# Kernel optimization log

Hardware: AMD Instinct MI355X
Metric: run time of the kernel (lower is better)

Reference implementation:

```python
import jax, jax.numpy as jnp
import numpy as np

N_NODES, N_EDGES, IN_F = 20000, 320000, 64
H1, H2 = 2, 2          # attn heads per GATv2 layer
D1, D2 = 128, 128      # gnn_size per layer
NM = [128, 128]        # nodemlp hidden sizes
EM = [512, 256]        # edgemlp hidden sizes
OUT_F = 1
NEG_SLOPE = 0.2


def _lin_init(key, fan_in, fan_out):
    kw, kb = jax.random.split(key)
    s = 1.0 / np.sqrt(fan_in)
    return (jax.random.uniform(kw, (fan_in, fan_out), jnp.float32, -s, s),
            jax.random.uniform(kb, (fan_out,), jnp.float32, -s, s))


def setup_inputs() -> dict:
    key = jax.random.key(0)
    ks = jax.random.split(key, 16)
    x = jax.random.normal(ks[0], (N_NODES, IN_F), jnp.float32)
    src = jax.random.randint(ks[1], (N_EDGES,), 0, N_NODES, jnp.int32)
    dst = jax.random.randint(ks[2], (N_EDGES,), 0, N_NODES, jnp.int32)
    # NodeMLP
    nw0, nb0 = _lin_init(ks[3], IN_F, NM[0])
    nw1, nb1 = _lin_init(ks[4], NM[0], NM[1])
    # GATv2 layer 1 (in=IN_F -> H1*D1)
    g1ws, g1bs = _lin_init(ks[5], IN_F, H1 * D1)
    g1wd, g1bd = _lin_init(ks[6], IN_F, H1 * D1)
    g1a = jax.random.normal(ks[7], (H1, D1), jnp.float32) * (1.0 / np.sqrt(D1))
    # GATv2 layer 2 (in=H1*D1 -> H2*D2)
    g2ws, g2bs = _lin_init(ks[8], H1 * D1, H2 * D2)
    g2wd, g2bd = _lin_init(ks[9], H1 * D1, H2 * D2)
    g2a = jax.random.normal(ks[10], (H2, D2), jnp.float32) * (1.0 / np.sqrt(D2))
    # EdgeMLP: in = 2*(NM[-1] + H2*D2) = 768
    e_in = 2 * (NM[-1] + H2 * D2)
    ew0, eb0 = _lin_init(ks[11], e_in, EM[0])
    ew1, eb1 = _lin_init(ks[12], EM[0], EM[1])
    ew2, eb2 = _lin_init(ks[13], EM[1], OUT_F)
    return dict(x=x, src=src, dst=dst,
                nw0=nw0, nb0=nb0, nw1=nw1, nb1=nb1,
                g1ws=g1ws, g1bs=g1bs, g1wd=g1wd, g1bd=g1bd, g1a=g1a,
                g2ws=g2ws, g2bs=g2bs, g2wd=g2wd, g2bd=g2bd, g2a=g2a,
                ew0=ew0, eb0=eb0, ew1=ew1, eb1=eb1, ew2=ew2, eb2=eb2)


def _segment_softmax(logits, dst, n):
    # logits: (E, H); softmax over edges sharing the same dst node
    m = jax.ops.segment_max(logits, dst, num_segments=n)
    e = jnp.exp(logits - m[dst])
    s = jax.ops.segment_sum(e, dst, num_segments=n)
    return e / s[dst]


def _gatv2(h, src, dst, ws, bs, wd, bd, attn, heads, dim, n):
    fs = (h @ ws + bs).reshape(n, heads, dim)   # fc_src
    fd = (h @ wd + bd).reshape(n, heads, dim)   # fc_dst
    e = jax.nn.leaky_relu(fs[src] + fd[dst], NEG_SLOPE)      # (E,H,D)
    logits = jnp.einsum('ehd,hd->eh', e, attn)               # (E,H)
    a = _segment_softmax(logits, dst, n)                      # (E,H)
    out = jax.ops.segment_sum(a[..., None] * fs[src], dst, num_segments=n)
    return jax.nn.relu(out).reshape(n, heads * dim)           # flatten heads


def reference(x, src, dst,
              nw0, nb0, nw1, nb1,
              g1ws, g1bs, g1wd, g1bd, g1a,
              g2ws, g2bs, g2wd, g2bd, g2a,
              ew0, eb0, ew1, eb1, ew2, eb2):
    n = x.shape[0]
    # NodeMLP (dropout=0 -> identity)
    h1 = jax.nn.relu(x @ nw0 + nb0)
    h1 = jax.nn.relu(h1 @ nw1 + nb1)
    # GCN: two GATv2Conv layers with relu activation, heads flattened
    h2 = _gatv2(x, src, dst, g1ws, g1bs, g1wd, g1bd, g1a, H1, D1, n)
    h2 = _gatv2(h2, src, dst, g2ws, g2bs, g2wd, g2bd, g2a, H2, D2, n)
    # EdgeMLP: gather src/dst, concat, MLP (relu before every layer but first)
    h = jnp.concatenate([h1[src], h1[dst], h2[src], h2[dst]], axis=1)  # (E,768)
    h = h @ ew0 + eb0
    h = jax.nn.relu(h) @ ew1 + eb1
    h = jax.nn.relu(h) @ ew2 + eb2
    return h  # (E, 1) edge scores
```

## Files before the change

### kernel.cpp

```cpp
#include <hip/hip_runtime.h>
#include <hip/hip_bf16.h>

constexpr int N_NODES = 20000;
constexpr int N_EDGES = 320000;

typedef _Float16 half8 __attribute__((ext_vector_type(8)));
typedef _Float16 half4 __attribute__((ext_vector_type(4)));
typedef float    f32x16 __attribute__((ext_vector_type(16)));

__device__ __forceinline__ float lrelu(float x) { return x > 0.f ? x : 0.2f * x; }

__global__ void hist_kernel(const int* __restrict__ dst, int* __restrict__ counts) {
    int e = blockIdx.x * 256 + threadIdx.x;
    if (e < N_EDGES) atomicAdd(&counts[dst[e]], 1);
}

__global__ void scan_all_kernel(const int* __restrict__ counts,
                                int* __restrict__ row_off, int* __restrict__ cursor) {
    __shared__ int ps[1024];
    const int t = threadIdx.x;
    const int base = t * 20;
    int loc[20];
    int sum = 0;
#pragma unroll
    for (int i = 0; i < 20; ++i) {
        const int idx = base + i;
        const int v = (idx < N_NODES) ? counts[idx] : 0;
        loc[i] = sum;
        sum += v;
    }
    ps[t] = sum;
    __syncthreads();
    for (int off = 1; off < 1024; off <<= 1) {
        const int v = (t >= off) ? ps[t - off] : 0;
        __syncthreads();
        ps[t] += v;
        __syncthreads();
    }
    const int ex = ps[t] - sum;
#pragma unroll
    for (int i = 0; i < 20; ++i) {
        const int idx = base + i;
        if (idx < N_NODES) {
            row_off[idx] = ex + loc[i];
            cursor[idx]  = ex + loc[i];
        }
    }
    if (t == 0) row_off[N_NODES] = N_EDGES;
}

__global__ void scatter_kernel(const int* __restrict__ src, const int* __restrict__ dst,
                               int* __restrict__ cursor, int* __restrict__ eidx,
                               int* __restrict__ srcs) {
    int e = blockIdx.x * 256 + threadIdx.x;
    if (e < N_EDGES) {
        int p = atomicAdd(&cursor[dst[e]], 1);
        eidx[p] = e;
        srcs[p] = src[e];
    }
}

template <int K, int M>
__device__ __forceinline__ void pack_one(int idx, const float* __restrict__ W,
                                         int r1, int k1, int r2, int joff, int ldw,
                                         _Float16* __restrict__ H,
                                         _Float16* __restrict__ L) {
    const int l  = idx & 63;
    const int t  = (idx >> 6) % (M / 32);
    const int s  = (idx >> 6) / (M / 32);
    const int j  = joff + t * 32 + (l & 31);
    const int kb = s * 16 + (l >> 5) * 8;
    half8 vh, vl;
#pragma unroll
    for (int i = 0; i < 8; ++i) {
        const int k    = kb + i;
        const int rrow = (k < k1) ? (r1 + k) : (r2 + (k - k1));
        const float w  = W[(size_t)rrow * ldw + j];
        const _Float16 h = (_Float16)w;
        vh[i] = h;
        vl[i] = (_Float16)(w - (float)h);
    }
    reinterpret_cast<half8*>(H)[idx] = vh;
    reinterpret_cast<half8*>(L)[idx] = vl;
}

constexpr int OFF_W1  = 0;
constexpr int OFF_G1S = 16384;
constexpr int OFF_G1D = 18432;
constexpr int OFF_G2S = 20480;
constexpr int OFF_G2D = 28672;
constexpr int OFF_SW0 = 36864;
constexpr int OFF_SW1 = 49152;
constexpr int OFF_DW0 = 61440;
constexpr int OFF_DW1 = 73728;
constexpr int OFF_N0  = 86016;
constexpr int OFF_N1  = 87040;
constexpr int PACK_TOT = 89088;

struct PackIn {
    const float *ew1, *g1ws, *g1wd, *g2ws, *g2wd, *ew0, *nw0, *nw1;
    _Float16 *H, *L;
};

__global__ void prepack_all_kernel(PackIn a) {
    const int idx = blockIdx.x * 256 + threadIdx.x;
    if (idx >= PACK_TOT) return;
    _Float16* H = a.H;
    _Float16* L = a.L;
    if (idx < OFF_G1S)
        pack_one<512, 256>(idx - OFF_W1, a.ew1, 0, 512, 0, 0, 256,
                           H + OFF_W1 * 8, L + OFF_W1 * 8);
    else if (idx < OFF_G1D)
        pack_one<64, 256>(idx - OFF_G1S, a.g1ws, 0, 64, 0, 0, 256,
                          H + OFF_G1S * 8, L + OFF_G1S * 8);
    else if (idx < OFF_G2S)
        pack_one<64, 256>(idx - OFF_G1D, a.g1wd, 0, 64, 0, 0, 256,
                          H + OFF_G1D * 8, L + OFF_G1D * 8);
    else if (idx < OFF_G2D)
        pack_one<256, 256>(idx - OFF_G2S, a.g2ws, 0, 256, 0, 0, 256,
                           H + OFF_G2S * 8, L + OFF_G2S * 8);
    else if (idx < OFF_SW0)
        pack_one<256, 256>(idx - OFF_G2D, a.g2wd, 0, 256, 0, 0, 256,
                           H + OFF_G2D * 8, L + OFF_G2D * 8);
    else if (idx < OFF_SW1)
        pack_one<384, 256>(idx - OFF_SW0, a.ew0, 0, 128, 256, 0, 512,
                           H + OFF_SW0 * 8, L + OFF_SW0 * 8);
    else if (idx < OFF_DW0)
        pack_one<384, 256>(idx - OFF_SW1, a.ew0, 0, 128, 256, 256, 512,
                           H + OFF_SW1 * 8, L + OFF_SW1 * 8);
    else if (idx < OFF_DW1)
        pack_one<384, 256>(idx - OFF_DW0, a.ew0, 128, 128, 512, 0, 512,
                           H + OFF_DW0 * 8, L + OFF_DW0 * 8);
    else if (idx < OFF_N0)
        pack_one<384, 256>(idx - OFF_DW1, a.ew0, 128, 128, 512, 256, 512,
                           H + OFF_DW1 * 8, L + OFF_DW1 * 8);
    else if (idx < OFF_N1)
        pack_one<64, 128>(idx - OFF_N0, a.nw0, 0, 64, 0, 0, 128,
                          H + OFF_N0 * 8, L + OFF_N0 * 8);
    else
        pack_one<128, 128>(idx - OFF_N1, a.nw1, 0, 128, 0, 0, 128,
                           H + OFF_N1 * 8, L + OFF_N1 * 8);
}

struct LinOut { float* y[4]; const float* b[4]; _Float16* yh[4]; };

template <int K, int TJ, int WR, int K1, int LD1, int LD2, int LDY,
          bool RELU, int MINW, int SEG>
__global__ __launch_bounds__(256, MINW) void mfma_linear2_kernel(
    const float* __restrict__ X1, const float* __restrict__ X2,
    const _Float16* __restrict__ BHp, const _Float16* __restrict__ BLp,
    LinOut lo, int N) {
    constexpr int WC    = 4 / WR;
    constexpr int TILES = WC * TJ;
    const int jb  = blockIdx.y;
    const int tid = threadIdx.x;
    const int wv  = tid >> 6, l = tid & 63;
    const int rg  = (WR == 1) ? 0 : ((WR == 4) ? wv : (wv & 1));
    const int cg  = (WR == 1) ? wv : ((WR == 4) ? 0 : (wv >> 1));
    const int m   = l & 31, h = l >> 5;
    const int row = blockIdx.x * (32 * WR) + rg * 32 + m;
    const int ar  = (row < N) ? row : (N - 1);
    const float* __restrict__ xr1 = X1 + (size_t)ar * LD1;
    const float* __restrict__ xr2 = X2 + (size_t)ar * LD2;
    const half8* __restrict__ BH = reinterpret_cast<const half8*>(BHp) + (size_t)jb * SEG;
    const half8* __restrict__ BL = reinterpret_cast<const half8*>(BLp) + (size_t)jb * SEG;
    const float* __restrict__ bp = lo.b[jb];
    float* __restrict__ Y = lo.y[jb];
    _Float16* __restrict__ Yh = lo.yh[jb];

    f32x16 acc[TJ];
#pragma unroll
    for (int jt = 0; jt < TJ; ++jt) {
        const float bv = bp ? bp[cg * TJ * 32 + jt * 32 + m] : 0.f;
#pragma unroll
        for (int r = 0; r < 16; ++r) acc[jt][r] = bv;
    }

    const int kf = h * 8;
    const float* pf = (kf < K1) ? (xr1 + kf) : (xr2 + (kf - K1));
    float4 xa = *reinterpret_cast<const float4*>(pf);
    float4 xb = *reinterpret_cast<const float4*>(pf + 4);

    for (int s = 0; s < K / 16; ++s) {
        const float xs[8] = {xa.x, xa.y, xa.z, xa.w, xb.x, xb.y, xb.z, xb.w};
        if (s + 1 < K / 16) {
            const int kn = (s + 1) * 16 + h * 8;
            const float* pn = (kn < K1) ? (xr1 + kn) : (xr2 + (kn - K1));
            xa = *reinterpret_cast<const float4*>(pn);
            xb = *reinterpret_cast<const float4*>(pn + 4);
        }
        half8 ah, al;
#pragma unroll
        for (int i = 0; i < 8; ++i) {
            const _Float16 hi = (_Float16)xs[i];
            ah[i] = hi;
            al[i] = (_Float16)(xs[i] - (float)hi);
        }
#pragma unroll
        for (int jt = 0; jt < TJ; ++jt) {
            const int fi = (s * TILES + cg * TJ + jt) * 64 + l;
            const half8 bh = BH[fi];
            const half8 bl = BL[fi];
            acc[jt] = __builtin_amdgcn_mfma_f32_32x32x16_f16(ah, bh, acc[jt], 0, 0, 0);
            acc[jt] = __builtin_amdgcn_mfma_f32_32x32x16_f16(al, bh, acc[jt], 0, 0, 0);
            acc[jt] = __builtin_amdgcn_mfma_f32_32x32x16_f16(ah, bl, acc[jt], 0, 0, 0);
        }
    }

    const int rbase = blockIdx.x * (32 * WR) + rg * 32;
#pragma unroll
    for (int jt = 0; jt < TJ; ++jt) {
        const int j = cg * TJ * 32 + jt * 32 + m;
#pragma unroll
        for (int r = 0; r < 16; ++r) {
            const int orow = rbase + (r & 3) + 8 * (r >> 2) + 4 * h;
            if (orow < N) {
                float v = acc[jt][r];
                if (RELU) v = fmaxf(v, 0.f);
                if (Y)  Y[(size_t)orow * LDY + j] = v;
                if (Yh) Yh[(size_t)orow * LDY + j] = (_Float16)v;
            }
        }
    }
}

__global__ void gat_fused_kernel(const _Float16* __restrict__ fsh,
                                 const float* __restrict__ fd,
                                 const float* __restrict__ attn,
                                 const int* __restrict__ row_off,
                                 const int* __restrict__ srcs,
                                 float* __restrict__ outp) {
    const int wv = threadIdx.x >> 6, l = threadIdx.x & 63;
    const int n = blockIdx.x * 4 + wv;
    if (n >= N_NODES) return;
    const int base = (l >> 5) * 128 + (l & 31) * 4;
    const float4 fdv = *reinterpret_cast<const float4*>(&fd[n * 256 + base]);
    const float4 av  = *reinterpret_cast<const float4*>(&attn[base]);
    const int s0 = row_off[n], s1 = row_off[n + 1];

    float m = -INFINITY, lsum = 0.f;
    float4 acc = {0.f, 0.f, 0.f, 0.f};
    half4 v0 = {0, 0, 0, 0}, v1 = {0, 0, 0, 0};
    if (s0 < s1)
        v0 = *reinterpret_cast<const half4*>(&fsh[(size_t)srcs[s0] * 256 + base]);
    if (s0 + 1 < s1)
        v1 = *reinterpret_cast<const half4*>(&fsh[(size_t)srcs[s0 + 1] * 256 + base]);
    for (int i = s0; i < s1; ++i) {
        const float4 vc = {(float)v0.x, (float)v0.y, (float)v0.z, (float)v0.w};
        v0 = v1;
        if (i + 2 < s1)
            v1 = *reinterpret_cast<const half4*>(&fsh[(size_t)srcs[i + 2] * 256 + base]);
        float p = lrelu(vc.x + fdv.x) * av.x;
        p = fmaf(lrelu(vc.y + fdv.y), av.y, p);
        p = fmaf(lrelu(vc.z + fdv.z), av.z, p);
        p = fmaf(lrelu(vc.w + fdv.w), av.w, p);
#pragma unroll
        for (int off = 1; off < 32; off <<= 1) p += __shfl_xor(p, off);
        const float mn = fmaxf(m, p);
        const float alpha = __expf(m - mn);
        const float w = __expf(p - mn);
        lsum = fmaf(lsum, alpha, w);
        acc.x = fmaf(acc.x, alpha, w * vc.x);
        acc.y = fmaf(acc.y, alpha, w * vc.y);
        acc.z = fmaf(acc.z, alpha, w * vc.z);
        acc.w = fmaf(acc.w, alpha, w * vc.w);
        m = mn;
    }
    const float inv = (s1 > s0) ? 1.f / lsum : 0.f;
    float4 o;
    o.x = fmaxf(acc.x * inv, 0.f);
    o.y = fmaxf(acc.y * inv, 0.f);
    o.z = fmaxf(acc.z * inv, 0.f);
    o.w = fmaxf(acc.w * inv, 0.f);
    *reinterpret_cast<float4*>(&outp[n * 256 + base]) = o;
}

__global__ __launch_bounds__(256, 2) void edge_mlp7_kernel(
    const _Float16* __restrict__ S, const _Float16* __restrict__ Dn,
    const int* __restrict__ srcs, const int* __restrict__ eidx,
    const int* __restrict__ dstf,
    const _Float16* __restrict__ WpH,
    const float* __restrict__ b1, const float* __restrict__ w2,
    const float* __restrict__ b2, float* __restrict__ out) {
    __shared__ __align__(16) _Float16 Bs[2][8][512];
    const int tid = threadIdx.x;
    const int wv  = tid >> 6, l = tid & 63;
    const int m   = l & 31, h = l >> 5;
    const int e0  = blockIdx.x * 128;
    const int slot = e0 + wv * 32 + m;
    const _Float16* __restrict__ Srow = S  + (size_t)srcs[slot] * 512;
    const _Float16* __restrict__ Drow = Dn + (size_t)dstf[eidx[slot]] * 512;

    f32x16 acc[8];
#pragma unroll
    for (int jt = 0; jt < 8; ++jt) {
        const float bv = b1[jt * 32 + m];
#pragma unroll
        for (int r = 0; r < 16; ++r) acc[jt][r] = bv;
    }

#pragma unroll
    for (int c = 0; c < 2; ++c) {
        const int jt = wv * 2 + c;
        *reinterpret_cast<float4*>(&Bs[0][jt][l * 8]) =
            *reinterpret_cast<const float4*>(WpH + ((size_t)jt * 64 + l) * 8);
    }
    half8 sv = *reinterpret_cast<const half8*>(Srow + h * 8);
    half8 dv = *reinterpret_cast<const half8*>(Drow + h * 8);
    __syncthreads();

    for (int s = 0; s < 32; ++s) {
        const int buf = s & 1;
        float4 bst[2];
        if (s < 31) {
#pragma unroll
            for (int c = 0; c < 2; ++c) {
                const int jt = wv * 2 + c;
                bst[c] = *reinterpret_cast<const float4*>(
                    WpH + ((size_t)((s + 1) * 8 + jt) * 64 + l) * 8);
            }
        }
        half8 xh;
#pragma unroll
        for (int i = 0; i < 8; ++i) {
            const _Float16 t = sv[i] + dv[i];
            xh[i] = t > (_Float16)0.f ? t : (_Float16)0.f;
        }
        if (s < 31) {
            const int ko = (s + 1) * 16 + h * 8;
            sv = *reinterpret_cast<const half8*>(Srow + ko);
            dv = *reinterpret_cast<const half8*>(Drow + ko);
        }
#pragma unroll
        for (int jt = 0; jt < 8; ++jt) {
            const half8 bh = *reinterpret_cast<const half8*>(&Bs[buf][jt][l * 8]);
            acc[jt] = __builtin_amdgcn_mfma_f32_32x32x16_f16(xh, bh, acc[jt], 0, 0, 0);
        }
        if (s < 31) {
#pragma unroll
            for (int c = 0; c < 2; ++c) {
                const int jt = wv * 2 + c;
                *reinterpret_cast<float4*>(&Bs[buf ^ 1][jt][l * 8]) = bst[c];
            }
        }
        __syncthreads();
    }

    float part[16];
#pragma unroll
    for (int r = 0; r < 16; ++r) part[r] = 0.f;
#pragma unroll
    for (int jt = 0; jt < 8; ++jt) {
        const float w2v = w2[jt * 32 + m];
#pragma unroll
        for (int r = 0; r < 16; ++r)
            part[r] = fmaf(fmaxf(acc[jt][r], 0.f), w2v, part[r]);
    }
#pragma unroll
    for (int off = 1; off < 32; off <<= 1)
#pragma unroll
        for (int r = 0; r < 16; ++r) part[r] += __shfl_xor(part[r], off);
    if (m == 0) {
        const float b2v = b2[0];
#pragma unroll
        for (int r = 0; r < 16; ++r) {
            const int row = (r & 3) + 8 * (r >> 2) + 4 * h;
            out[eidx[e0 + wv * 32 + row]] = part[r] + b2v;
        }
    }
}

extern "C" void kernel_launch(void* const* d_in, const int* in_sizes, int n_in,
                              void* d_out, int out_size, void* d_ws, size_t ws_size,
                              hipStream_t stream) {
    (void)in_sizes; (void)n_in; (void)out_size; (void)ws_size;
    const float* x    = (const float*)d_in[0];
    const int*   src  = (const int*)d_in[1];
    const int*   dst  = (const int*)d_in[2];
    const float* nw0  = (const float*)d_in[3];
    const float* nb0  = (const float*)d_in[4];
    const float* nw1  = (const float*)d_in[5];
    const float* nb1  = (const float*)d_in[6];
    const float* g1ws = (const float*)d_in[7];
    const float* g1bs = (const float*)d_in[8];
    const float* g1wd = (const float*)d_in[9];
    const float* g1bd = (const float*)d_in[10];
    const float* g1a  = (const float*)d_in[11];
    const float* g2ws = (const float*)d_in[12];
    const float* g2bs = (const float*)d_in[13];
    const float* g2wd = (const float*)d_in[14];
    const float* g2bd = (const float*)d_in[15];
    const float* g2a  = (const float*)d_in[16];
    const float* ew0  = (const float*)d_in[17];
    const float* eb0  = (const float*)d_in[18];
    const float* ew1  = (const float*)d_in[19];
    const float* eb1  = (const float*)d_in[20];
    const float* ew2  = (const float*)d_in[21];
    const float* eb2  = (const float*)d_in[22];
    float* out = (float*)d_out;

    float* wsF = (float*)d_ws;
    float* h1  = wsF;
    float* g2o = wsF + 2560000;
    float* fsb = wsF + 7680000;
    float* fdb = wsF + 12800000;
    float* g1o = wsF + 17920000;
    _Float16* Sh = (_Float16*)(wsF + 7680000);
    _Float16* Dh = (_Float16*)(wsF + 12800000);
    _Float16* fsh = (_Float16*)(wsF + 23040000);
    int* wsI     = (int*)(wsF + 28160000);
    int* row_off = wsI;
    int* cursor  = wsI + 20016;
    int* eidx    = wsI + 40032;
    int* srcs    = wsI + 360032;
    _Float16* pkH = (_Float16*)((char*)d_ws + 115361280);
    _Float16* pkL = pkH + (size_t)PACK_TOT * 8;

    hipMemsetAsync(cursor, 0, N_NODES * sizeof(int), stream);
    hist_kernel<<<1250, 256, 0, stream>>>(dst, cursor);
    scan_all_kernel<<<1, 1024, 0, stream>>>(cursor, row_off, cursor);
    scatter_kernel<<<1250, 256, 0, stream>>>(src, dst, cursor, eidx, srcs);

    PackIn pin{ew1, g1ws, g1wd, g2ws, g2wd, ew0, nw0, nw1, pkH, pkL};
    prepack_all_kernel<<<(PACK_TOT + 255) / 256, 256, 0, stream>>>(pin);

    {   LinOut lo{{fsb, nullptr, nullptr, nullptr}, {nb0, nullptr, nullptr, nullptr},
                  {nullptr, nullptr, nullptr, nullptr}};
        mfma_linear2_kernel<64, 1, 1, 64, 64, 64, 128, true, 4, 0>
            <<<dim3(625, 1), 256, 0, stream>>>(x, x, pkH + OFF_N0 * 8, pkL + OFF_N0 * 8,
                                               lo, N_NODES); }
    {   LinOut lo{{h1, nullptr, nullptr, nullptr}, {nb1, nullptr, nullptr, nullptr},
                  {nullptr, nullptr, nullptr, nullptr}};
        mfma_linear2_kernel<128, 1, 1, 128, 128, 128, 128, true, 4, 0>
            <<<dim3(625, 1), 256, 0, stream>>>(fsb, fsb, pkH + OFF_N1 * 8, pkL + OFF_N1 * 8,
                                               lo, N_NODES); }

    {   LinOut lo{{nullptr, fdb, nullptr, nullptr}, {g1bs, g1bd, nullptr, nullptr},
                  {fsh, nullptr, nullptr, nullptr}};
        mfma_linear2_kernel<64, 2, 1, 64, 64, 64, 256, false, 4, 2048>
            <<<dim3(625, 2), 256, 0, stream>>>(x, x, pkH + OFF_G1S * 8, pkL + OFF_G1S * 8,
                                               lo, N_NODES); }
    gat_fused_kernel<<<5000, 256, 0, stream>>>(fsh, fdb, g1a, row_off, srcs, g1o);

    {   LinOut lo{{nullptr, fdb, nullptr, nullptr}, {g2bs, g2bd, nullptr, nullptr},
                  {fsh, nullptr, nullptr, nullptr}};
        mfma_linear2_kernel<256, 8, 4, 256, 256, 256, 256, false, 2, 8192>
            <<<dim3(157, 2), 256, 0, stream>>>(g1o, g1o, pkH + OFF_G2S * 8, pkL + OFF_G2S * 8,
                                               lo, N_NODES); }
    gat_fused_kernel<<<5000, 256, 0, stream>>>(fsh, fdb, g2a, row_off, srcs, g2o);

    {   LinOut lo{{nullptr, nullptr, nullptr, nullptr}, {nullptr, nullptr, eb0, eb0 + 256},
                  {Sh, Sh + 256, Dh, Dh + 256}};
        mfma_linear2_kernel<384, 8, 4, 128, 128, 256, 512, false, 2, 12288>
            <<<dim3(157, 4), 256, 0, stream>>>(h1, g2o, pkH + OFF_SW0 * 8, pkL + OFF_SW0 * 8,
                                               lo, N_NODES); }

    edge_mlp7_kernel<<<N_EDGES / 128, 256, 0, stream>>>(Sh, Dh, srcs, eidx, dst,
                                                        pkH + OFF_W1 * 8,
                                                        eb1, ew2, eb2, out);
}
```

Baseline: 542.4 us.

## Merge input-x linears, unroll GAT edge loop by two, stream edge-MLP weights via registers

```diff
diff --git a/kernel.cpp b/kernel.cpp
--- a/kernel.cpp
+++ b/kernel.cpp
@@ -85,16 +85,14 @@
 }
 
 constexpr int OFF_W1  = 0;
-constexpr int OFF_G1S = 16384;
-constexpr int OFF_G1D = 18432;
-constexpr int OFF_G2S = 20480;
-constexpr int OFF_G2D = 28672;
-constexpr int OFF_SW0 = 36864;
-constexpr int OFF_SW1 = 49152;
-constexpr int OFF_DW0 = 61440;
-constexpr int OFF_DW1 = 73728;
-constexpr int OFF_N0  = 86016;
-constexpr int OFF_N1  = 87040;
+constexpr int OFF_G2S = 16384;
+constexpr int OFF_G2D = 24576;
+constexpr int OFF_SW0 = 32768;
+constexpr int OFF_SW1 = 45056;
+constexpr int OFF_DW0 = 57344;
+constexpr int OFF_DW1 = 69632;
+constexpr int OFF_N1  = 81920;
+constexpr int OFF_X   = 83968;
 constexpr int PACK_TOT = 89088;
 
 struct PackIn {
@@ -107,15 +105,9 @@
     if (idx >= PACK_TOT) return;
     _Float16* H = a.H;
     _Float16* L = a.L;
-    if (idx < OFF_G1S)
+    if (idx < OFF_G2S)
         pack_one<512, 256>(idx - OFF_W1, a.ew1, 0, 512, 0, 0, 256,
                            H + OFF_W1 * 8, L + OFF_W1 * 8);
-    else if (idx < OFF_G1D)
-        pack_one<64, 256>(idx - OFF_G1S, a.g1ws, 0, 64, 0, 0, 256,
-                          H + OFF_G1S * 8, L + OFF_G1S * 8);
-    else if (idx < OFF_G2S)
-        pack_one<64, 256>(idx - OFF_G1D, a.g1wd, 0, 64, 0, 0, 256,
-                          H + OFF_G1D * 8, L + OFF_G1D * 8);
     else if (idx < OFF_G2D)
         pack_one<256, 256>(idx - OFF_G2S, a.g2ws, 0, 256, 0, 0, 256,
                            H + OFF_G2S * 8, L + OFF_G2S * 8);
@@ -131,21 +123,30 @@
     else if (idx < OFF_DW1)
         pack_one<384, 256>(idx - OFF_DW0, a.ew0, 128, 128, 512, 0, 512,
                            H + OFF_DW0 * 8, L + OFF_DW0 * 8);
-    else if (idx < OFF_N0)
+    else if (idx < OFF_N1)
         pack_one<384, 256>(idx - OFF_DW1, a.ew0, 128, 128, 512, 256, 512,
                            H + OFF_DW1 * 8, L + OFF_DW1 * 8);
-    else if (idx < OFF_N1)
-        pack_one<64, 128>(idx - OFF_N0, a.nw0, 0, 64, 0, 0, 128,
-                          H + OFF_N0 * 8, L + OFF_N0 * 8);
-    else
+    else if (idx < OFF_X)
         pack_one<128, 128>(idx - OFF_N1, a.nw1, 0, 128, 0, 0, 128,
                            H + OFF_N1 * 8, L + OFF_N1 * 8);
-}
-
-struct LinOut { float* y[4]; const float* b[4]; _Float16* yh[4]; };
-
-template <int K, int TJ, int WR, int K1, int LD1, int LD2, int LDY,
-          bool RELU, int MINW, int SEG>
+    else {
+        const int xi  = idx - OFF_X;
+        const int seg = xi >> 10, r = xi & 1023;
+        const int sb  = OFF_X + seg * 1024;
+        if (seg == 0)
+            pack_one<64, 128>(r, a.nw0, 0, 64, 0, 0, 128, H + sb * 8, L + sb * 8);
+        else if (seg <= 2)
+            pack_one<64, 128>(r, a.g1ws, 0, 64, 0, (seg - 1) * 128, 256,
+                              H + sb * 8, L + sb * 8);
+        else
+            pack_one<64, 128>(r, a.g1wd, 0, 64, 0, (seg - 3) * 128, 256,
+                              H + sb * 8, L + sb * 8);
+    }
+}
+
+struct LinOut { float* y[6]; const float* b[6]; _Float16* yh[6]; int ldy[6]; int relu[6]; };
+
+template <int K, int TJ, int WR, int K1, int LD1, int LD2, int MINW, int SEG>
 __global__ __launch_bounds__(256, MINW) void mfma_linear2_kernel(
     const float* __restrict__ X1, const float* __restrict__ X2,
     const _Float16* __restrict__ BHp, const _Float16* __restrict__ BLp,
@@ -167,6 +168,8 @@
     const float* __restrict__ bp = lo.b[jb];
     float* __restrict__ Y = lo.y[jb];
     _Float16* __restrict__ Yh = lo.yh[jb];
+    const int ldy = lo.ldy[jb];
+    const int rel = lo.relu[jb];
 
     f32x16 acc[TJ];
 #pragma unroll
@@ -216,9 +219,9 @@
             const int orow = rbase + (r & 3) + 8 * (r >> 2) + 4 * h;
             if (orow < N) {
                 float v = acc[jt][r];
-                if (RELU) v = fmaxf(v, 0.f);
-                if (Y)  Y[(size_t)orow * LDY + j] = v;
-                if (Yh) Yh[(size_t)orow * LDY + j] = (_Float16)v;
+                if (rel) v = fmaxf(v, 0.f);
+                if (Y)  Y[(size_t)orow * ldy + j] = v;
+                if (Yh) Yh[(size_t)orow * ldy + j] = (_Float16)v;
             }
         }
     }
@@ -238,33 +241,61 @@
     const float4 av  = *reinterpret_cast<const float4*>(&attn[base]);
     const int s0 = row_off[n], s1 = row_off[n + 1];
 
+    auto LD = [&](int k) {
+        return *reinterpret_cast<const half4*>(&fsh[(size_t)srcs[k] * 256 + base]);
+    };
+    auto LOGIT = [&](const float4& v) {
+        float p = lrelu(v.x + fdv.x) * av.x;
+        p = fmaf(lrelu(v.y + fdv.y), av.y, p);
+        p = fmaf(lrelu(v.z + fdv.z), av.z, p);
+        p = fmaf(lrelu(v.w + fdv.w), av.w, p);
+        return p;
+    };
+
     float m = -INFINITY, lsum = 0.f;
     float4 acc = {0.f, 0.f, 0.f, 0.f};
-    half4 v0 = {0, 0, 0, 0}, v1 = {0, 0, 0, 0};
-    if (s0 < s1)
-        v0 = *reinterpret_cast<const half4*>(&fsh[(size_t)srcs[s0] * 256 + base]);
-    if (s0 + 1 < s1)
-        v1 = *reinterpret_cast<const half4*>(&fsh[(size_t)srcs[s0 + 1] * 256 + base]);
-    for (int i = s0; i < s1; ++i) {
-        const float4 vc = {(float)v0.x, (float)v0.y, (float)v0.z, (float)v0.w};
-        v0 = v1;
-        if (i + 2 < s1)
-            v1 = *reinterpret_cast<const half4*>(&fsh[(size_t)srcs[i + 2] * 256 + base]);
-        float p = lrelu(vc.x + fdv.x) * av.x;
-        p = fmaf(lrelu(vc.y + fdv.y), av.y, p);
-        p = fmaf(lrelu(vc.z + fdv.z), av.z, p);
-        p = fmaf(lrelu(vc.w + fdv.w), av.w, p);
-#pragma unroll
-        for (int off = 1; off < 32; off <<= 1) p += __shfl_xor(p, off);
-        const float mn = fmaxf(m, p);
+    half4 c0 = {0, 0, 0, 0}, c1 = {0, 0, 0, 0}, n0 = {0, 0, 0, 0}, n1 = {0, 0, 0, 0};
+    int i = s0;
+    if (i     < s1) c0 = LD(i);
+    if (i + 1 < s1) c1 = LD(i + 1);
+    if (i + 2 < s1) n0 = LD(i + 2);
+    if (i + 3 < s1) n1 = LD(i + 3);
+    for (; i + 1 < s1; i += 2) {
+        const float4 v0 = {(float)c0.x, (float)c0.y, (float)c0.z, (float)c0.w};
+        const float4 v1 = {(float)c1.x, (float)c1.y, (float)c1.z, (float)c1.w};
+        c0 = n0; c1 = n1;
+        if (i + 4 < s1) n0 = LD(i + 4);
+        if (i + 5 < s1) n1 = LD(i + 5);
+        float p0 = LOGIT(v0);
+        float p1 = LOGIT(v1);
+#pragma unroll
+        for (int off = 1; off < 32; off <<= 1) {
+            p0 += __shfl_xor(p0, off);
+            p1 += __shfl_xor(p1, off);
+        }
+        const float mn = fmaxf(m, fmaxf(p0, p1));
         const float alpha = __expf(m - mn);
-        const float w = __expf(p - mn);
-        lsum = fmaf(lsum, alpha, w);
-        acc.x = fmaf(acc.x, alpha, w * vc.x);
-        acc.y = fmaf(acc.y, alpha, w * vc.y);
-        acc.z = fmaf(acc.z, alpha, w * vc.z);
-        acc.w = fmaf(acc.w, alpha, w * vc.w);
+        const float w0 = __expf(p0 - mn), w1 = __expf(p1 - mn);
+        lsum = fmaf(lsum, alpha, w0 + w1);
+        acc.x = fmaf(w1, v1.x, fmaf(w0, v0.x, acc.x * alpha));
+        acc.y = fmaf(w1, v1.y, fmaf(w0, v0.y, acc.y * alpha));
+        acc.z = fmaf(w1, v1.z, fmaf(w0, v0.z, acc.z * alpha));
+        acc.w = fmaf(w1, v1.w, fmaf(w0, v0.w, acc.w * alpha));
         m = mn;
+    }
+    if (i < s1) {
+        const float4 v0 = {(float)c0.x, (float)c0.y, (float)c0.z, (float)c0.w};
+        float p0 = LOGIT(v0);
+#pragma unroll
+        for (int off = 1; off < 32; off <<= 1) p0 += __shfl_xor(p0, off);
+        const float mn = fmaxf(m, p0);
+        const float alpha = __expf(m - mn);
+        const float w0 = __expf(p0 - mn);
+        lsum = fmaf(lsum, alpha, w0);
+        acc.x = fmaf(w0, v0.x, acc.x * alpha);
+        acc.y = fmaf(w0, v0.y, acc.y * alpha);
+        acc.z = fmaf(w0, v0.z, acc.z * alpha);
+        acc.w = fmaf(w0, v0.w, acc.w * alpha);
     }
     const float inv = (s1 > s0) ? 1.f / lsum : 0.f;
     float4 o;
@@ -275,14 +306,13 @@
     *reinterpret_cast<float4*>(&outp[n * 256 + base]) = o;
 }
 
-__global__ __launch_bounds__(256, 2) void edge_mlp7_kernel(
+__global__ __launch_bounds__(256, 2) void edge_mlp8_kernel(
     const _Float16* __restrict__ S, const _Float16* __restrict__ Dn,
     const int* __restrict__ srcs, const int* __restrict__ eidx,
     const int* __restrict__ dstf,
     const _Float16* __restrict__ WpH,
     const float* __restrict__ b1, const float* __restrict__ w2,
     const float* __restrict__ b2, float* __restrict__ out) {
-    __shared__ __align__(16) _Float16 Bs[2][8][512];
     const int tid = threadIdx.x;
     const int wv  = tid >> 6, l = tid & 63;
     const int m   = l & 31, h = l >> 5;
@@ -290,6 +320,7 @@
     const int slot = e0 + wv * 32 + m;
     const _Float16* __restrict__ Srow = S  + (size_t)srcs[slot] * 512;
     const _Float16* __restrict__ Drow = Dn + (size_t)dstf[eidx[slot]] * 512;
+    const half8* __restrict__ Bp = reinterpret_cast<const half8*>(WpH);
 
     f32x16 acc[8];
 #pragma unroll
@@ -299,51 +330,48 @@
         for (int r = 0; r < 16; ++r) acc[jt][r] = bv;
     }
 
-#pragma unroll
-    for (int c = 0; c < 2; ++c) {
-        const int jt = wv * 2 + c;
-        *reinterpret_cast<float4*>(&Bs[0][jt][l * 8]) =
-            *reinterpret_cast<const float4*>(WpH + ((size_t)jt * 64 + l) * 8);
-    }
+    half8 bA[8], bB[8];
+#pragma unroll
+    for (int jt = 0; jt < 8; ++jt) bA[jt] = Bp[jt * 64 + l];
     half8 sv = *reinterpret_cast<const half8*>(Srow + h * 8);
     half8 dv = *reinterpret_cast<const half8*>(Drow + h * 8);
-    __syncthreads();
-
-    for (int s = 0; s < 32; ++s) {
-        const int buf = s & 1;
-        float4 bst[2];
-        if (s < 31) {
-#pragma unroll
-            for (int c = 0; c < 2; ++c) {
-                const int jt = wv * 2 + c;
-                bst[c] = *reinterpret_cast<const float4*>(
-                    WpH + ((size_t)((s + 1) * 8 + jt) * 64 + l) * 8);
-            }
-        }
+
+    for (int s = 0; s < 32; s += 2) {
         half8 xh;
 #pragma unroll
         for (int i = 0; i < 8; ++i) {
             const _Float16 t = sv[i] + dv[i];
             xh[i] = t > (_Float16)0.f ? t : (_Float16)0.f;
         }
-        if (s < 31) {
+        {
             const int ko = (s + 1) * 16 + h * 8;
             sv = *reinterpret_cast<const half8*>(Srow + ko);
             dv = *reinterpret_cast<const half8*>(Drow + ko);
         }
 #pragma unroll
-        for (int jt = 0; jt < 8; ++jt) {
-            const half8 bh = *reinterpret_cast<const half8*>(&Bs[buf][jt][l * 8]);
-            acc[jt] = __builtin_amdgcn_mfma_f32_32x32x16_f16(xh, bh, acc[jt], 0, 0, 0);
-        }
-        if (s < 31) {
-#pragma unroll
-            for (int c = 0; c < 2; ++c) {
-                const int jt = wv * 2 + c;
-                *reinterpret_cast<float4*>(&Bs[buf ^ 1][jt][l * 8]) = bst[c];
-            }
-        }
-        __syncthreads();
+        for (int jt = 0; jt < 8; ++jt)
+            bB[jt] = Bp[(size_t)((s + 1) * 8 + jt) * 64 + l];
+#pragma unroll
+        for (int jt = 0; jt < 8; ++jt)
+            acc[jt] = __builtin_amdgcn_mfma_f32_32x32x16_f16(xh, bA[jt], acc[jt], 0, 0, 0);
+
+        half8 xh2;
+#pragma unroll
+        for (int i = 0; i < 8; ++i) {
+            const _Float16 t = sv[i] + dv[i];
+            xh2[i] = t > (_Float16)0.f ? t : (_Float16)0.f;
+        }
+        if (s + 2 < 32) {
+            const int ko = (s + 2) * 16 + h * 8;
+            sv = *reinterpret_cast<const half8*>(Srow + ko);
+            dv = *reinterpret_cast<const half8*>(Drow + ko);
+#pragma unroll
+            for (int jt = 0; jt < 8; ++jt)
+                bA[jt] = Bp[(size_t)((s + 2) * 8 + jt) * 64 + l];
+        }
+#pragma unroll
+        for (int jt = 0; jt < 8; ++jt)
+            acc[jt] = __builtin_amdgcn_mfma_f32_32x32x16_f16(xh2, bB[jt], acc[jt], 0, 0, 0);
     }
 
     float part[16];
@@ -424,38 +452,42 @@
     PackIn pin{ew1, g1ws, g1wd, g2ws, g2wd, ew0, nw0, nw1, pkH, pkL};
     prepack_all_kernel<<<(PACK_TOT + 255) / 256, 256, 0, stream>>>(pin);
 
-    {   LinOut lo{{fsb, nullptr, nullptr, nullptr}, {nb0, nullptr, nullptr, nullptr},
-                  {nullptr, nullptr, nullptr, nullptr}};
-        mfma_linear2_kernel<64, 1, 1, 64, 64, 64, 128, true, 4, 0>
-            <<<dim3(625, 1), 256, 0, stream>>>(x, x, pkH + OFF_N0 * 8, pkL + OFF_N0 * 8,
+    {   LinOut lo{};
+        lo.y[0] = fsb;        lo.b[0] = nb0;        lo.ldy[0] = 128; lo.relu[0] = 1;
+        lo.yh[1] = fsh;       lo.b[1] = g1bs;       lo.ldy[1] = 256;
+        lo.yh[2] = fsh + 128; lo.b[2] = g1bs + 128; lo.ldy[2] = 256;
+        lo.y[3] = fdb;        lo.b[3] = g1bd;       lo.ldy[3] = 256;
+        lo.y[4] = fdb + 128;  lo.b[4] = g1bd + 128; lo.ldy[4] = 256;
+        mfma_linear2_kernel<64, 1, 1, 64, 64, 64, 4, 1024>
+            <<<dim3(625, 5), 256, 0, stream>>>(x, x, pkH + OFF_X * 8, pkL + OFF_X * 8,
                                                lo, N_NODES); }
-    {   LinOut lo{{h1, nullptr, nullptr, nullptr}, {nb1, nullptr, nullptr, nullptr},
-                  {nullptr, nullptr, nullptr, nullptr}};
-        mfma_linear2_kernel<128, 1, 1, 128, 128, 128, 128, true, 4, 0>
+
+    {   LinOut lo{};
+        lo.y[0] = h1; lo.b[0] = nb1; lo.ldy[0] = 128; lo.relu[0] = 1;
+        mfma_linear2_kernel<128, 1, 1, 128, 128, 128, 4, 0>
             <<<dim3(625, 1), 256, 0, stream>>>(fsb, fsb, pkH + OFF_N1 * 8, pkL + OFF_N1 * 8,
                                                lo, N_NODES); }
 
-    {   LinOut lo{{nullptr, fdb, nullptr, nullptr}, {g1bs, g1bd, nullptr, nullptr},
-                  {fsh, nullptr, nullptr, nullptr}};
-        mfma_linear2_kernel<64, 2, 1, 64, 64, 64, 256, false, 4, 2048>
-            <<<dim3(625, 2), 256, 0, stream>>>(x, x, pkH + OFF_G1S * 8, pkL + OFF_G1S * 8,
-                                               lo, N_NODES); }
     gat_fused_kernel<<<5000, 256, 0, stream>>>(fsh, fdb, g1a, row_off, srcs, g1o);
 
-    {   LinOut lo{{nullptr, fdb, nullptr, nullptr}, {g2bs, g2bd, nullptr, nullptr},
-                  {fsh, nullptr, nullptr, nullptr}};
-        mfma_linear2_kernel<256, 8, 4, 256, 256, 256, 256, false, 2, 8192>
+    {   LinOut lo{};
+        lo.yh[0] = fsh; lo.b[0] = g2bs; lo.ldy[0] = 256;
+        lo.y[1] = fdb;  lo.b[1] = g2bd; lo.ldy[1] = 256;
+        mfma_linear2_kernel<256, 8, 4, 256, 256, 256, 2, 8192>
             <<<dim3(157, 2), 256, 0, stream>>>(g1o, g1o, pkH + OFF_G2S * 8, pkL + OFF_G2S * 8,
                                                lo, N_NODES); }
     gat_fused_kernel<<<5000, 256, 0, stream>>>(fsh, fdb, g2a, row_off, srcs, g2o);
 
-    {   LinOut lo{{nullptr, nullptr, nullptr, nullptr}, {nullptr, nullptr, eb0, eb0 + 256},
-                  {Sh, Sh + 256, Dh, Dh + 256}};
-        mfma_linear2_kernel<384, 8, 4, 128, 128, 256, 512, false, 2, 12288>
+    {   LinOut lo{};
+        lo.yh[0] = Sh;       lo.ldy[0] = 512;
+        lo.yh[1] = Sh + 256; lo.ldy[1] = 512;
+        lo.yh[2] = Dh;       lo.b[2] = eb0;       lo.ldy[2] = 512;
+        lo.yh[3] = Dh + 256; lo.b[3] = eb0 + 256; lo.ldy[3] = 512;
+        mfma_linear2_kernel<384, 8, 4, 128, 128, 256, 2, 12288>
             <<<dim3(157, 4), 256, 0, stream>>>(h1, g2o, pkH + OFF_SW0 * 8, pkL + OFF_SW0 * 8,
                                                lo, N_NODES); }
 
-    edge_mlp7_kernel<<<N_EDGES / 128, 256, 0, stream>>>(Sh, Dh, srcs, eidx, dst,
+    edge_mlp8_kernel<<<N_EDGES / 128, 256, 0, stream>>>(Sh, Dh, srcs, eidx, dst,
                                                         pkH + OFF_W1 * 8,
                                                         eb1, ew2, eb2, out);
 }
```

New measurement: 571.3 us. 5.3% more time.
